# Kernel optimization log

Measured on AMD Instinct MI355X. Metric: run time of the kernel, lower is better.

## Reference

```python
import jax, jax.numpy as jnp
import numpy as np
import math

B, T, C = 2, 2048, 2048
N_HEAD = 16
N_KV = 4
GROUP = N_HEAD // N_KV
HS = C // N_HEAD
WINDOW = 1024
SINK = 4


def setup_inputs() -> dict:
    key = jax.random.key(0)
    ks = jax.random.split(key, 5)
    s = 1.0 / math.sqrt(C)
    return {
        "x": jax.random.normal(ks[0], (B, T, C), dtype=jnp.float32),
        "Wq": jax.random.normal(ks[1], (C, C), dtype=jnp.float32) * s,
        "Wk": jax.random.normal(ks[2], (N_KV * HS, C), dtype=jnp.float32) * s,
        "Wv": jax.random.normal(ks[3], (N_KV * HS, C), dtype=jnp.float32) * s,
        "Wo": jax.random.normal(ks[4], (C, C), dtype=jnp.float32) * s,
    }


def _sliding_window_sink_mask(t):
    i = jnp.arange(t)[:, None]  # query index
    j = jnp.arange(t)[None, :]  # key index
    causal = j <= i
    band = j >= i - (WINDOW - 1)
    mask = causal & band
    mask = mask | (j < SINK)          # sink columns always visible
    mask = mask & ((i >= SINK) | causal)  # sink rows stay strictly causal
    return mask  # (T, T) bool


def reference(x, Wq, Wk, Wv, Wo):
    b, t, c = x.shape
    q = (x @ Wq.T).reshape(b, t, N_HEAD, HS).transpose(0, 2, 1, 3)
    # group q heads by kv head: (B, n_kv, group, T, hs)
    q = q.reshape(b, N_KV, GROUP, t, HS)
    k = (x @ Wk.T).reshape(b, t, N_KV, HS).transpose(0, 2, 1, 3)  # (B, n_kv, T, hs)
    v = (x @ Wv.T).reshape(b, t, N_KV, HS).transpose(0, 2, 1, 3)
    scale = 1.0 / math.sqrt(HS)
    # scores over full TxT (faithful to original, K/V expansion done via broadcast)
    att = jnp.einsum('bkgqd,bkjd->bkgqj', q, k) * scale
    mask = _sliding_window_sink_mask(t)  # (T, T)
    att = jnp.where(mask[None, None, None, :, :], att, -jnp.inf)
    att = jax.nn.softmax(att, axis=-1)
    y = jnp.einsum('bkgqj,bkjd->bkgqd', att, v)
    y = y.reshape(b, N_HEAD, t, HS).transpose(0, 2, 1, 3).reshape(b, t, c)
    return y @ Wo.T
```

## Files before the change

kernel.cpp:

```cpp
#include <hip/hip_runtime.h>


#define T_SEQ 2048
#define NKV   4
#define HS    128
#define CDIM  2048
#define QKVN  3072
#define WIN   1024
#define SINKN 4
#define PSTR  68

typedef __bf16 bf16x8 __attribute__((ext_vector_type(8)));
typedef float  f32x4  __attribute__((ext_vector_type(4)));

#define MFMA16(A, B, C) __builtin_amdgcn_mfma_f32_16x16x32_bf16(A, B, C, 0, 0, 0)
#define EXP2(x) __builtin_amdgcn_exp2f(x)

__device__ inline unsigned short f2bu(float f) {
  unsigned int u = __float_as_uint(f);
  u += 0x7fffu + ((u >> 16) & 1u);
  return (unsigned short)(u >> 16);
}
__device__ inline unsigned int pkhi(float f0, float f1) {
  return __builtin_amdgcn_perm(__float_as_uint(f1), __float_as_uint(f0),
                               0x07060302u);
}
__device__ inline __bf16 us2b(unsigned short u) {
  union { unsigned short u; __bf16 b; } t; t.u = u; return t.b;
}
__device__ inline f32x4 fzero4() { f32x4 z = {0.f, 0.f, 0.f, 0.f}; return z; }

__device__ __forceinline__ void glds16(const void* g, const void* lds_uniform) {
  typedef __attribute__((address_space(1))) void gv;
  typedef __attribute__((address_space(3))) void lv;
  __builtin_amdgcn_global_load_lds((gv*)(unsigned long long)g,
                                   (lv*)(unsigned int)(unsigned long long)lds_uniform,
                                   16, 0, 0);
}

#define SZ_X  8388608
#define SZ_WQ 4194304
#define SZ_WK 1048576
#define OFF_WQ (SZ_X)
#define OFF_WK (SZ_X + SZ_WQ)
#define OFF_WV (OFF_WK + SZ_WK)
#define OFF_WO (OFF_WV + SZ_WK)
#define SZ_ALL (OFF_WO + SZ_WQ)

__global__ __launch_bounds__(256) void f2b_all(const float* __restrict__ x,
                                               const float* __restrict__ wq,
                                               const float* __restrict__ wk,
                                               const float* __restrict__ wv,
                                               const float* __restrict__ wo,
                                               unsigned short* __restrict__ out,
                                               float qs) {
  int i = (blockIdx.x * 256 + threadIdx.x) * 4;
  const float* src; int off; float sc = 1.0f;
  if (i < OFF_WQ)      { src = x;  off = 0; }
  else if (i < OFF_WK) { src = wq; off = OFF_WQ; sc = qs; }
  else if (i < OFF_WV) { src = wk; off = OFF_WK; }
  else if (i < OFF_WO) { src = wv; off = OFF_WV; }
  else                 { src = wo; off = OFF_WO; }
  float4 v = *reinterpret_cast<const float4*>(src + (i - off));
  ushort4 o;
  o.x = f2bu(v.x * sc); o.y = f2bu(v.y * sc);
  o.z = f2bu(v.z * sc); o.w = f2bu(v.w * sc);
  *reinterpret_cast<ushort4*>(out + i) = o;
}

__device__ inline void storeC(unsigned short* p, float v) { *p = f2bu(v); }
__device__ inline void storeC(float* p, float v) { *p = v; }

template <typename OutT>
__global__ __launch_bounds__(256) void gemm_abt(const unsigned short* __restrict__ A,
                                                const unsigned short* __restrict__ B,
                                                OutT* __restrict__ C,
                                                int M, int N, int K) {
  __shared__ __align__(16) unsigned short As[128 * 32];
  __shared__ __align__(16) unsigned short Bs[128 * 32];
  const int tid  = threadIdx.x;
  const int wave = tid >> 6, lane = tid & 63;
  const int quad = lane >> 4, l16 = lane & 15;
  const int wm = (wave >> 1) * 64, wn = (wave & 1) * 64;
  const int tm = blockIdx.x * 128, tn = blockIdx.y * 128;

  f32x4 acc[4][4];
#pragma unroll
  for (int i = 0; i < 4; ++i)
#pragma unroll
    for (int j = 0; j < 4; ++j) acc[i][j] = fzero4();

  for (int k0 = 0; k0 < K; k0 += 32) {
    __syncthreads();
#pragma unroll
    for (int it = 0; it < 2; ++it) {
      int chunk = wave * 2 + it;
      int f = (chunk * 64 + lane) * 8;
      int r = f >> 5, c = f & 31;
      glds16(&A[(size_t)(tm + r) * K + k0 + c], &As[chunk * 512]);
      glds16(&B[(size_t)(tn + r) * K + k0 + c], &Bs[chunk * 512]);
    }
    __syncthreads();
    bf16x8 af[4], bfr[4];
#pragma unroll
    for (int i = 0; i < 4; ++i) {
      af[i]  = *reinterpret_cast<const bf16x8*>(&As[(wm + i * 16 + l16) * 32 + quad * 8]);
      bfr[i] = *reinterpret_cast<const bf16x8*>(&Bs[(wn + i * 16 + l16) * 32 + quad * 8]);
    }
#pragma unroll
    for (int i = 0; i < 4; ++i)
#pragma unroll
      for (int j = 0; j < 4; ++j) acc[i][j] = MFMA16(af[i], bfr[j], acc[i][j]);
  }
#pragma unroll
  for (int i = 0; i < 4; ++i)
#pragma unroll
    for (int j = 0; j < 4; ++j)
#pragma unroll
      for (int r = 0; r < 4; ++r) {
        int row = tm + wm + i * 16 + quad * 4 + r;
        int col = tn + wn + j * 16 + l16;
        storeC(&C[(size_t)row * N + col], acc[i][j][r]);
      }
}

__global__ __launch_bounds__(256) void kvpack(const unsigned short* __restrict__ QKV,
                                              unsigned short* __restrict__ Kp,
                                              unsigned short* __restrict__ Vp) {
  const int tid  = threadIdx.x;
  const int kt64 = blockIdx.x;
  const int bk   = blockIdx.y;
  const int b = bk >> 2, kvh = bk & 3;
  const int kt = kt64 * 64;
  const int bT = b * T_SEQ;
  const int dq = tid & 15;

  unsigned short* kdst = &Kp[(size_t)(bk * 32 + kt64) * 8192];
#pragma unroll
  for (int it = 0; it < 4; ++it) {
    int key = it * 16 + (tid >> 4);
    float4 v = *reinterpret_cast<const float4*>(
        &QKV[(size_t)(bT + kt + key) * QKVN + 2048 + kvh * HS + dq * 8]);
    int c = dq >> 2, quad = dq & 3, nt = key & 3, l16s = key >> 2;
    *reinterpret_cast<float4*>(
        &kdst[((size_t)((c * 4 + nt) * 64 + quad * 16 + l16s)) * 8]) = v;
  }

#pragma unroll
  for (int it = 0; it < 4; ++it) {
    int key = it * 16 + (tid >> 4);
    float4 v = *reinterpret_cast<const float4*>(
        &QKV[(size_t)(bT + kt + key) * QKVN + 2560 + kvh * HS + dq * 8]);
    const unsigned short* pv = reinterpret_cast<const unsigned short*>(&v);
    int kt32 = kt64 * 2 + (key >> 5);
    int quad = (key & 31) >> 3, j = key & 7;
    unsigned short* vdst = &Vp[(size_t)(bk * 64 + kt32) * 4096];
#pragma unroll
    for (int j2 = 0; j2 < 8; ++j2) {
      int d = dq * 8 + j2, dt = d >> 4, l16v = d & 15;
      vdst[((size_t)(dt * 64 + quad * 16 + l16v)) * 8 + j] = pv[j2];
    }
  }
}

__global__ __launch_bounds__(256) void attn_kernel(const unsigned short* __restrict__ QKV,
                                                   const unsigned short* __restrict__ Kp,
                                                   const unsigned short* __restrict__ Vp,
                                                   unsigned short* __restrict__ Y) {
  __shared__ __align__(16) unsigned short KVs[16384];
  __shared__ __align__(16) unsigned short Ps[4 * 32 * PSTR];
  unsigned short* Ks = KVs;
  unsigned short* Vs = KVs + 8192;

  const int tid  = threadIdx.x;
  const int wave = tid >> 6, lane = tid & 63;
  const int quad = lane >> 4, l16 = lane & 15;
  const int qt0 = (int)(gridDim.x - 1 - blockIdx.x) * 32;
  const int kvh = blockIdx.y, b = blockIdx.z;
  const int h   = kvh * 4 + wave;
  const int bk  = b * NKV + kvh;
  const int bT  = b * T_SEQ;
  unsigned short* Pw = &Ps[wave * 32 * PSTR];

  bf16x8 qa[2][4];
#pragma unroll
  for (int mt = 0; mt < 2; ++mt)
#pragma unroll
    for (int c = 0; c < 4; ++c)
      qa[mt][c] = *reinterpret_cast<const bf16x8*>(
          &QKV[(size_t)(bT + qt0 + mt * 16 + l16) * QKVN + h * HS + c * 32 + quad * 8]);

  bf16x8 ones;
#pragma unroll
  for (int j = 0; j < 8; ++j) ones[j] = us2b(0x3F80);

  f32x4 o[2][9];
#pragma unroll
  for (int mt = 0; mt < 2; ++mt)
#pragma unroll
    for (int dt = 0; dt < 9; ++dt) o[mt][dt] = fzero4();

  const int start = (qt0 >= 1024) ? ((qt0 - 1023) & ~63) : 0;
  const int sink  = (start > 0) ? 1 : 0;
  const int nch   = ((qt0 + 32 - start + 63) >> 6) + sink;

  for (int ci = 0; ci < nch; ++ci) {
    const bool is_sink = (sink && ci == 0);
    const int  kt  = is_sink ? 0 : start + (ci - sink) * 64;
    const int  rem = qt0 + 32 - kt;
    const int  kcmax = is_sink ? 1 : (rem >= 64 ? 2 : ((rem + 31) >> 5));
    const bool full  = !is_sink && (kt + 63 <= qt0) && (kt >= qt0 - 992);

    __syncthreads();
    {
      const unsigned short* kg = &Kp[(size_t)(bk * 32 + (kt >> 6)) * 8192 + lane * 8];
      const unsigned short* vg = &Vp[(size_t)(bk * 64 + (kt >> 5)) * 4096 + lane * 8];
#pragma unroll
      for (int i = 0; i < 4; ++i) {
        int part = wave * 4 + i;
        glds16(kg + part * 512, &Ks[part * 512]);
        glds16(vg + part * 512, &Vs[part * 512]);
      }
    }
    __syncthreads();

    f32x4 s[2][4];
#pragma unroll
    for (int nt = 0; nt < 4; ++nt) { s[0][nt] = fzero4(); s[1][nt] = fzero4(); }
#pragma unroll
    for (int c = 0; c < 4; ++c) {
#pragma unroll
      for (int nt = 0; nt < 4; ++nt) {
        bf16x8 kf = *reinterpret_cast<const bf16x8*>(&Ks[(c * 4 + nt) * 512 + lane * 8]);
        s[0][nt] = MFMA16(qa[0][c], kf, s[0][nt]);
        s[1][nt] = MFMA16(qa[1][c], kf, s[1][nt]);
      }
    }

    if (full) {
#pragma unroll
      for (int mt = 0; mt < 2; ++mt)
#pragma unroll
        for (int r = 0; r < 4; ++r) {
          const int row = mt * 16 + quad * 4 + r;
          uint2 pk;
          pk.x = pkhi(EXP2(s[mt][0][r]), EXP2(s[mt][1][r]));
          pk.y = pkhi(EXP2(s[mt][2][r]), EXP2(s[mt][3][r]));
          *reinterpret_cast<uint2*>(&Pw[row * PSTR + l16 * 4]) = pk;
        }
    } else {
#pragma unroll
      for (int mt = 0; mt < 2; ++mt)
#pragma unroll
        for (int r = 0; r < 4; ++r) {
          const int row = mt * 16 + quad * 4 + r;
          const int qi  = qt0 + row;
          float p[4];
#pragma unroll
          for (int nt = 0; nt < 4; ++nt) {
            int kj = kt + l16 * 4 + nt;
            bool ok = ((kj <= qi) && (kj + (WIN - 1) >= qi)) ||
                      ((kj < SINKN) && (qi >= SINKN));
            p[nt] = ok ? EXP2(s[mt][nt][r]) : 0.f;
          }
          uint2 pk;
          pk.x = pkhi(p[0], p[1]);
          pk.y = pkhi(p[2], p[3]);
          *reinterpret_cast<uint2*>(&Pw[row * PSTR + l16 * 4]) = pk;
        }
    }
    asm volatile("s_waitcnt lgkmcnt(0)" ::: "memory");

#pragma unroll
    for (int kc = 0; kc < 2; ++kc)
      if (kc < kcmax) {
#pragma unroll
        for (int mt = 0; mt < 2; ++mt) {
          bf16x8 pf = *reinterpret_cast<const bf16x8*>(
              &Pw[(mt * 16 + l16) * PSTR + kc * 32 + quad * 8]);
#pragma unroll
          for (int dt = 0; dt < 8; ++dt) {
            bf16x8 vf = *reinterpret_cast<const bf16x8*>(
                &Vs[kc * 4096 + dt * 512 + lane * 8]);
            o[mt][dt] = MFMA16(pf, vf, o[mt][dt]);
          }
          o[mt][8] = MFMA16(pf, ones, o[mt][8]);
        }
      }
  }

  __syncthreads();
  unsigned short* Yst = KVs;
#pragma unroll
  for (int mt = 0; mt < 2; ++mt) {
    float inv[4];
#pragma unroll
    for (int r = 0; r < 4; ++r) inv[r] = __builtin_amdgcn_rcpf(o[mt][8][r]);
#pragma unroll
    for (int dt = 0; dt < 8; ++dt)
#pragma unroll
      for (int r = 0; r < 4; ++r)
        Yst[(mt * 16 + quad * 4 + r) * 512 + wave * 128 + dt * 16 + l16] =
            f2bu(o[mt][dt][r] * inv[r]);
  }
  __syncthreads();
#pragma unroll
  for (int it = 0; it < 8; ++it) {
    int idx = it * 256 + tid;
    int row = idx >> 6, col = (idx & 63) * 8;
    *reinterpret_cast<uint4*>(
        &Y[(size_t)(bT + qt0 + row) * CDIM + kvh * 512 + col]) =
        *reinterpret_cast<const uint4*>(&Yst[row * 512 + col]);
  }
}

extern "C" void kernel_launch(void* const* d_in, const int* in_sizes, int n_in,
                              void* d_out, int out_size, void* d_ws, size_t ws_size,
                              hipStream_t stream) {
  const float* x  = (const float*)d_in[0];
  const float* Wq = (const float*)d_in[1];
  const float* Wk = (const float*)d_in[2];
  const float* Wv = (const float*)d_in[3];
  const float* Wo = (const float*)d_in[4];
  float* out = (float*)d_out;

  unsigned short* base = (unsigned short*)d_ws;
  unsigned short* xb   = base;
  unsigned short* wqb  = xb + OFF_WQ;
  unsigned short* wob  = xb + OFF_WO;
  unsigned short* QKVb = xb + SZ_ALL;
  unsigned short* Kpb  = wqb;
  unsigned short* Vpb  = wqb + 2097152;
  unsigned short* Yb   = xb;

  const float qscale = 0.08838834764831845f * 1.4426950408889634f;
  f2b_all<<<SZ_ALL / 1024, 256, 0, stream>>>(x, Wq, Wk, Wv, Wo, xb, qscale);

  gemm_abt<unsigned short><<<dim3(32, 24), 256, 0, stream>>>(xb, wqb, QKVb, 4096, QKVN, 2048);

  kvpack<<<dim3(32, 8), 256, 0, stream>>>(QKVb, Kpb, Vpb);

  attn_kernel<<<dim3(64, 4, 2), 256, 0, stream>>>(QKVb, Kpb, Vpb, Yb);

  gemm_abt<float><<<dim3(32, 16), 256, 0, stream>>>(Yb, wob, out, 4096, 2048, 2048);
}
```

Baseline: 298.7 us.

## Replace GEMM with 256x256 double-buffered, swizzled LDS pipelined MFMA kernel

Replaces the simple 128x128, K=32 single-buffered GEMM with a 256x256 tile, K=64, 8-wave kernel. It double-buffers LDS and interleaves global-to-LDS prefetch of the next K tile with MFMA phases, using manual waitcnt and barriers plus s_setprio. The LDS layout gets an XOR swizzle against bank conflicts, and the block index is remapped for L2 locality. The aim is to cut per-iteration sync stalls and global-load latency exposure in both projection GEMMs. The cost is heavy register and LDS use (128KB LDS across two buffers) and fragile hand-written wait-count logic.

```diff
diff --git a/kernel.cpp b/kernel.cpp
--- a/kernel.cpp
+++ b/kernel.cpp
@@ -72,55 +72,141 @@
 __device__ inline void storeC(float* p, float v) { *p = v; }
 
 template <typename OutT>
-__global__ __launch_bounds__(256) void gemm_abt(const unsigned short* __restrict__ A,
-                                                const unsigned short* __restrict__ B,
-                                                OutT* __restrict__ C,
-                                                int M, int N, int K) {
-  __shared__ __align__(16) unsigned short As[128 * 32];
-  __shared__ __align__(16) unsigned short Bs[128 * 32];
+__global__ __launch_bounds__(512, 2) void gemm256(const unsigned short* __restrict__ A,
+                                                  const unsigned short* __restrict__ B,
+                                                  OutT* __restrict__ C,
+                                                  int M, int N, int K) {
+  __shared__ __align__(16) unsigned short As[2][16384];
+  __shared__ __align__(16) unsigned short Bs[2][16384];
   const int tid  = threadIdx.x;
   const int wave = tid >> 6, lane = tid & 63;
   const int quad = lane >> 4, l16 = lane & 15;
-  const int wm = (wave >> 1) * 64, wn = (wave & 1) * 64;
-  const int tm = blockIdx.x * 128, tn = blockIdx.y * 128;
-
-  f32x4 acc[4][4];
-#pragma unroll
-  for (int i = 0; i < 4; ++i)
+  const int wmi  = wave >> 2, wni = wave & 3;
+  const int sx   = ((l16 >> 2) & 1) << 5;
+
+  const int tmn  = M >> 8;
+  const int qq   = gridDim.x >> 3;
+  const int swzb = (blockIdx.x & 7) * qq + (blockIdx.x >> 3);
+  const int tm   = (swzb % tmn) << 8;
+  const int tn   = (swzb / tmn) << 8;
+
+  const int logl = (lane * 16) ^ (((lane >> 5) & 1) << 5);
+  const int srow = logl >> 7;
+  const int scol = (logl & 127) >> 1;
+  const int NT   = K >> 6;
+
+  auto issueA = [&](int tt, int ch) {
+    glds16(&A[(size_t)(tm + ch * 8 + srow) * K + (tt << 6) + scol],
+           (const char*)As + ((tt & 1) << 15) + ch * 1024);
+  };
+  auto issueB = [&](int tt, int ch) {
+    glds16(&B[(size_t)(tn + ch * 8 + srow) * K + (tt << 6) + scol],
+           (const char*)Bs + ((tt & 1) << 15) + ch * 1024);
+  };
+
+  f32x4 acc[8][4];
+#pragma unroll
+  for (int i = 0; i < 8; ++i)
 #pragma unroll
     for (int j = 0; j < 4; ++j) acc[i][j] = fzero4();
 
-  for (int k0 = 0; k0 < K; k0 += 32) {
-    __syncthreads();
-#pragma unroll
-    for (int it = 0; it < 2; ++it) {
-      int chunk = wave * 2 + it;
-      int f = (chunk * 64 + lane) * 8;
-      int r = f >> 5, c = f & 31;
-      glds16(&A[(size_t)(tm + r) * K + k0 + c], &As[chunk * 512]);
-      glds16(&B[(size_t)(tn + r) * K + k0 + c], &Bs[chunk * 512]);
-    }
-    __syncthreads();
-    bf16x8 af[4], bfr[4];
-#pragma unroll
-    for (int i = 0; i < 4; ++i) {
-      af[i]  = *reinterpret_cast<const bf16x8*>(&As[(wm + i * 16 + l16) * 32 + quad * 8]);
-      bfr[i] = *reinterpret_cast<const bf16x8*>(&Bs[(wn + i * 16 + l16) * 32 + quad * 8]);
-    }
-#pragma unroll
-    for (int i = 0; i < 4; ++i)
-#pragma unroll
-      for (int j = 0; j < 4; ++j) acc[i][j] = MFMA16(af[i], bfr[j], acc[i][j]);
-  }
-#pragma unroll
-  for (int i = 0; i < 4; ++i)
-#pragma unroll
-    for (int j = 0; j < 4; ++j)
+  issueB(0, wave); issueB(0, 8 + wave); issueB(0, 16 + wave); issueB(0, 24 + wave);
+  issueA(0, wave); issueA(0, 16 + wave); issueA(0, 8 + wave); issueA(0, 24 + wave);
+  if (NT > 1) {
+    issueB(1, wave); issueB(1, 8 + wave);
+    asm volatile("s_waitcnt vmcnt(2)" ::: "memory");
+  } else {
+    asm volatile("s_waitcnt vmcnt(0)" ::: "memory");
+  }
+  __builtin_amdgcn_s_barrier();
+
+#pragma unroll 2
+  for (int t = 0; t < NT; ++t) {
+    const char* Asc = (const char*)As + ((t & 1) << 15);
+    const char* Bsc = (const char*)Bs + ((t & 1) << 15);
+    const bool h1 = (t + 1 < NT), h2 = (t + 2 < NT);
+    bf16x8 aq[4], bq[4];
+
+#pragma unroll
+    for (int g = 0; g < 4; ++g)
+      bq[g] = *reinterpret_cast<const bf16x8*>(
+          Bsc + ((((wni * 64 + g * 16 + l16) << 7) + quad * 16) ^ sx));
+#pragma unroll
+    for (int f = 0; f < 4; ++f)
+      aq[f] = *reinterpret_cast<const bf16x8*>(
+          Asc + ((((wmi * 128 + f * 16 + l16) << 7) + quad * 16) ^ sx));
+    if (h1) { issueB(t + 1, 16 + wave); issueB(t + 1, 24 + wave); }
+    __builtin_amdgcn_s_barrier();
+    asm volatile("s_waitcnt lgkmcnt(0)" ::: "memory");
+    __builtin_amdgcn_s_setprio(1);
+#pragma unroll
+    for (int f = 0; f < 4; ++f)
+#pragma unroll
+      for (int g = 0; g < 4; ++g) acc[f][g] = MFMA16(aq[f], bq[g], acc[f][g]);
+    __builtin_amdgcn_s_setprio(0);
+    __builtin_amdgcn_s_barrier();
+
+#pragma unroll
+    for (int f = 0; f < 4; ++f)
+      aq[f] = *reinterpret_cast<const bf16x8*>(
+          Asc + ((((wmi * 128 + 64 + f * 16 + l16) << 7) + quad * 16) ^ sx));
+    if (h1) { issueA(t + 1, wave); issueA(t + 1, 16 + wave); }
+    __builtin_amdgcn_s_barrier();
+    asm volatile("s_waitcnt lgkmcnt(0)" ::: "memory");
+    __builtin_amdgcn_s_setprio(1);
+#pragma unroll
+    for (int f = 0; f < 4; ++f)
+#pragma unroll
+      for (int g = 0; g < 4; ++g) acc[4 + f][g] = MFMA16(aq[f], bq[g], acc[4 + f][g]);
+    __builtin_amdgcn_s_setprio(0);
+    __builtin_amdgcn_s_barrier();
+
+#pragma unroll
+    for (int g = 0; g < 4; ++g)
+      bq[g] = *reinterpret_cast<const bf16x8*>(
+          Bsc + ((((wni * 64 + g * 16 + l16) << 7) + 64 + quad * 16) ^ sx));
+#pragma unroll
+    for (int f = 0; f < 4; ++f)
+      aq[f] = *reinterpret_cast<const bf16x8*>(
+          Asc + ((((wmi * 128 + f * 16 + l16) << 7) + 64 + quad * 16) ^ sx));
+    if (h1) { issueA(t + 1, 8 + wave); issueA(t + 1, 24 + wave); }
+    __builtin_amdgcn_s_barrier();
+    asm volatile("s_waitcnt lgkmcnt(0)" ::: "memory");
+    __builtin_amdgcn_s_setprio(1);
+#pragma unroll
+    for (int f = 0; f < 4; ++f)
+#pragma unroll
+      for (int g = 0; g < 4; ++g) acc[f][g] = MFMA16(aq[f], bq[g], acc[f][g]);
+    __builtin_amdgcn_s_setprio(0);
+    __builtin_amdgcn_s_barrier();
+
+#pragma unroll
+    for (int f = 0; f < 4; ++f)
+      aq[f] = *reinterpret_cast<const bf16x8*>(
+          Asc + ((((wmi * 128 + 64 + f * 16 + l16) << 7) + 64 + quad * 16) ^ sx));
+    if (h2) { issueB(t + 2, wave); issueB(t + 2, 8 + wave); }
+    __builtin_amdgcn_s_barrier();
+    asm volatile("s_waitcnt lgkmcnt(0)" ::: "memory");
+    __builtin_amdgcn_s_setprio(1);
+#pragma unroll
+    for (int f = 0; f < 4; ++f)
+#pragma unroll
+      for (int g = 0; g < 4; ++g) acc[4 + f][g] = MFMA16(aq[f], bq[g], acc[4 + f][g]);
+    __builtin_amdgcn_s_setprio(0);
+    if (h2) asm volatile("s_waitcnt vmcnt(2)" ::: "memory");
+    else    asm volatile("s_waitcnt vmcnt(0)" ::: "memory");
+    __builtin_amdgcn_s_barrier();
+  }
+
+#pragma unroll
+  for (int fi = 0; fi < 8; ++fi)
+#pragma unroll
+    for (int g = 0; g < 4; ++g)
 #pragma unroll
       for (int r = 0; r < 4; ++r) {
-        int row = tm + wm + i * 16 + quad * 4 + r;
-        int col = tn + wn + j * 16 + l16;
-        storeC(&C[(size_t)row * N + col], acc[i][j][r]);
+        const int row = tm + wmi * 128 + fi * 16 + quad * 4 + r;
+        const int col = tn + wni * 64 + g * 16 + l16;
+        storeC(&C[(size_t)row * N + col], acc[fi][g][r]);
       }
 }
 
@@ -336,11 +422,11 @@
   const float qscale = 0.08838834764831845f * 1.4426950408889634f;
   f2b_all<<<SZ_ALL / 1024, 256, 0, stream>>>(x, Wq, Wk, Wv, Wo, xb, qscale);
 
-  gemm_abt<unsigned short><<<dim3(32, 24), 256, 0, stream>>>(xb, wqb, QKVb, 4096, QKVN, 2048);
+  gemm256<unsigned short><<<192, 512, 0, stream>>>(xb, wqb, QKVb, 4096, QKVN, 2048);
 
   kvpack<<<dim3(32, 8), 256, 0, stream>>>(QKVb, Kpb, Vpb);
 
   attn_kernel<<<dim3(64, 4, 2), 256, 0, stream>>>(QKVb, Kpb, Vpb, Yb);
 
-  gemm_abt<float><<<dim3(32, 16), 256, 0, stream>>>(Yb, wob, out, 4096, 2048, 2048);
-}
+  gemm256<float><<<128, 512, 0, stream>>>(Yb, wob, out, 4096, 2048, 2048);
+}
```

Measured after the change: 304.1 us. Within noise of the previous version (+1.8%).
